# Optimization experiments

Hardware: AMD Instinct MI355X
Metric: run time of the kernel (lower is better)

Reference implementation:

```python
import jax, jax.numpy as jnp
import numpy as np

NUM_HEADS = 12

def _pe(L, d):
    # standard sinusoidal positional encoding, shape (1, L, d)
    pos = jnp.arange(L, dtype=jnp.float32)[:, None]
    i = jnp.arange(d)[None, :]
    angle = pos / jnp.power(10000.0, (2 * (i // 2)).astype(jnp.float32) / d)
    pe = jnp.where(i % 2 == 0, jnp.sin(angle), jnp.cos(angle))
    return pe[None]

def _ln(x, scale, bias, eps=1e-5):
    m = x.mean(-1, keepdims=True)
    v = ((x - m) ** 2).mean(-1, keepdims=True)
    return (x - m) / jnp.sqrt(v + eps) * scale + bias

def setup_inputs() -> dict:
    key = jax.random.key(0)
    ks = jax.random.split(key, 8)
    D = 768
    s = 0.02
    return {
        "x": jax.random.normal(ks[0], (8, D, 32, 32), jnp.float32),
        "context_token": jax.random.normal(ks[1], (1, 1, D), jnp.float32),
        "register_tokens": jax.random.normal(ks[2], (1, 4, D), jnp.float32),
        "in_proj_w": jax.random.normal(ks[3], (3 * D, D), jnp.float32) * s,
        "in_proj_b": jnp.zeros((3 * D,), jnp.float32),
        "out_proj_w": jax.random.normal(ks[4], (D, D), jnp.float32) * s,
        "out_proj_b": jnp.zeros((D,), jnp.float32),
        "ln1_s": jnp.ones((D,), jnp.float32),
        "ln1_b": jnp.zeros((D,), jnp.float32),
        "ln2_s": jnp.ones((D,), jnp.float32),
        "ln2_b": jnp.zeros((D,), jnp.float32),
        "ffn_w1": jax.random.normal(ks[5], (4 * D, D), jnp.float32) * s,
        "ffn_b1": jnp.zeros((4 * D,), jnp.float32),
        "ffn_w2": jax.random.normal(ks[6], (D, 4 * D), jnp.float32) * s,
        "ffn_b2": jnp.zeros((D,), jnp.float32),
    }

def reference(x, context_token, register_tokens, in_proj_w, in_proj_b,
              out_proj_w, out_proj_b, ln1_s, ln1_b, ln2_s, ln2_b,
              ffn_w1, ffn_b1, ffn_w2, ffn_b2):
    B, d, h, w = x.shape
    N = h * w
    R = register_tokens.shape[1]
    G = 1 + R  # global tokens: context + registers
    nh = NUM_HEADS
    dh = d // nh
    # (B, N, d)
    x_flat = x.reshape(B, d, N).transpose(0, 2, 1)
    tokens = jnp.concatenate([
        jnp.broadcast_to(context_token, (B, 1, d)),
        jnp.broadcast_to(register_tokens, (B, R, d)),
    ], axis=1)
    tokens = tokens + _pe(G, d)
    xwt = _ln(jnp.concatenate([tokens, x_flat], axis=1), ln1_s, ln1_b)
    S = G + N
    # MultiheadAttention (eval mode, dropout off): fused in-projection
    qkv = xwt @ in_proj_w.T + in_proj_b
    q, k, v = jnp.split(qkv, 3, axis=-1)
    to_heads = lambda t: t.reshape(B, S, nh, dh).transpose(0, 2, 1, 3)
    q, k, v = to_heads(q), to_heads(k), to_heads(v)
    scores = jnp.einsum('bhqd,bhkd->bhqk', q, k) / np.float32(np.sqrt(dh))
    # mask (True = disallowed): feature rows (>=G) cannot attend to global cols (<G);
    # global rows attend everything; feature-feature block allowed.
    row_feat = jnp.arange(S) >= G
    col_glob = jnp.arange(S) < G
    disallowed = row_feat[:, None] & col_glob[None, :]
    scores = jnp.where(disallowed, -jnp.inf, scores)
    attn = jax.nn.softmax(scores, axis=-1)
    o = jnp.einsum('bhqk,bhkd->bhqd', attn, v).transpose(0, 2, 1, 3).reshape(B, S, d)
    o = o @ out_proj_w.T + out_proj_b
    y = o + xwt
    ff = jax.nn.gelu(_ln(y, ln2_s, ln2_b) @ ffn_w1.T + ffn_b1, approximate=False) @ ffn_w2.T + ffn_b2
    y = y + ff
    context_out = y[:, 0:1, :]
    register_out = y[:, 1:G, :]
    feature_out = y[:, G:, :].transpose(0, 2, 1).reshape(B, d, h, w)
    return feature_out, context_out, register_out
```

## Files before the change

kernel.cpp:

```cpp
#include <hip/hip_runtime.h>
#include <hip/hip_bf16.h>
#include <cmath>

typedef unsigned short u16;
typedef __bf16 bf16x8 __attribute__((ext_vector_type(8)));
typedef float floatx4 __attribute__((ext_vector_type(4)));

#define SQ 1029
#define DM 768
#define NH 12
#define SQP 1088
#define SSC 0.18033688011112042f

#define GLD16(gp, lp) __builtin_amdgcn_global_load_lds( \
    (const __attribute__((address_space(1))) unsigned int*)(gp), \
    (__attribute__((address_space(3))) unsigned int*)(lp), 16, 0, 0)

#define OFF_WQKV ((size_t)0)
#define OFF_WOUT ((size_t)3538944)
#define OFF_W1   ((size_t)4718592)
#define OFF_W2   ((size_t)9437184)
#define OFF_XF   ((size_t)14155776)
#define OFF_XWT  ((size_t)26800128)
#define OFF_QKV  ((size_t)39444480)
#define OFF_VT   ((size_t)77783040)
#define OFF_Y    ((size_t)91152384)
#define OFF_BQ   ((size_t)103796736)

__device__ __forceinline__ float bf2f(u16 u) {
  unsigned int x = ((unsigned int)u) << 16;
  float f; __builtin_memcpy(&f, &x, 4); return f;
}
__device__ __forceinline__ u16 f2bf(float f) {
  unsigned int x; __builtin_memcpy(&x, &f, 4);
  x = (x + 0x7fffu + ((x >> 16) & 1u)) >> 16;
  return (u16)x;
}
__device__ __forceinline__ unsigned int pk_bf16(float a, float b) {
  __hip_bfloat162 h = __float22bfloat162_rn(make_float2(a, b));
  unsigned int u; __builtin_memcpy(&u, &h, 4); return u;
}

__device__ __forceinline__ void blockReduce2(float& s1, float& s2) {
  #pragma unroll
  for (int o = 32; o > 0; o >>= 1) { s1 += __shfl_xor(s1, o); s2 += __shfl_xor(s2, o); }
  __shared__ float t1[4], t2[4];
  const int w = threadIdx.x >> 6;
  if ((threadIdx.x & 63) == 0) { t1[w] = s1; t2[w] = s2; }
  __syncthreads();
  s1 = t1[0] + t1[1] + t1[2] + t1[3];
  s2 = t2[0] + t2[1] + t2[2] + t2[3];
}

__global__ __launch_bounds__(256) void convw_all(
    const float* __restrict__ a, const float* __restrict__ b,
    const float* __restrict__ c, const float* __restrict__ d,
    const float* __restrict__ bq, u16* __restrict__ dst, float* __restrict__ bqs) {
  int i = blockIdx.x * 256 + threadIdx.x;
  if (i >= 1770048) return;
  if (i >= 1769472) {
    const int off = i - 1769472;
    float4 v = ((const float4*)bq)[off];
    if (off < 192) { v.x *= SSC; v.y *= SSC; v.z *= SSC; v.w *= SSC; }
    ((float4*)bqs)[off] = v;
    return;
  }
  const float* src; int off;
  if (i < 442368)       { src = a; off = i; }
  else if (i < 589824)  { src = b; off = i - 442368; }
  else if (i < 1179648) { src = c; off = i - 589824; }
  else                  { src = d; off = i - 1179648; }
  float4 v = ((const float4*)src)[off];
  if (i < 147456) { v.x *= SSC; v.y *= SSC; v.z *= SSC; v.w *= SSC; }
  ushort4 o; o.x = f2bf(v.x); o.y = f2bf(v.y); o.z = f2bf(v.z); o.w = f2bf(v.w);
  ((ushort4*)dst)[i] = o;
}

__global__ __launch_bounds__(256) void ln1_fused(
    const float* __restrict__ x, const float* __restrict__ ctx, const float* __restrict__ regt,
    const float* __restrict__ g, const float* __restrict__ be, u16* __restrict__ xwt) {
  const int bx = blockIdx.x;
  const int tid = threadIdx.x;
  if (bx >= 256) {
    const int row = bx - 256;
    const int b = row / 5, s = row % 5;
    float v[3];
    #pragma unroll
    for (int i = 0; i < 3; ++i) {
      const int c = tid + i * 256;
      float tok = (s == 0) ? ctx[c] : regt[(s - 1) * DM + c];
      float e = (float)(2 * (c / 2)) * (1.0f / 768.0f);
      float ang = (float)s / powf(10000.0f, e);
      v[i] = tok + ((c & 1) ? cosf(ang) : sinf(ang));
    }
    float s1 = v[0] + v[1] + v[2];
    float s2 = v[0] * v[0] + v[1] * v[1] + v[2] * v[2];
    blockReduce2(s1, s2);
    const float mean = s1 * (1.0f / 768.0f);
    const float var = s2 * (1.0f / 768.0f) - mean * mean;
    const float rs = rsqrtf(fmaxf(var, 0.0f) + 1e-5f);
    #pragma unroll
    for (int i = 0; i < 3; ++i) {
      const int c = tid + i * 256;
      xwt[((size_t)b * SQ + s) * DM + c] = f2bf((v[i] - mean) * rs * g[c] + be[c]);
    }
    return;
  }
  __shared__ u16 XT[32][772];
  const int b = bx >> 5, st = bx & 31;
  const int i2 = tid & 15, cj = tid >> 4;
  const int n0 = st * 32;
  #pragma unroll 4
  for (int ct = 0; ct < 48; ++ct) {
    const int c = ct * 16 + cj;
    const float2 v = *(const float2*)&x[((size_t)b * 768 + c) * 1024 + n0 + i2 * 2];
    XT[i2 * 2][c]     = f2bf(v.x);
    XT[i2 * 2 + 1][c] = f2bf(v.y);
  }
  __syncthreads();
  const int wave = tid >> 6, lane = tid & 63;
  float gr[12], br[12];
  #pragma unroll
  for (int k = 0; k < 12; ++k) { gr[k] = g[lane + k * 64]; br[k] = be[lane + k * 64]; }
  #pragma unroll
  for (int rr = 0; rr < 8; ++rr) {
    const int row = wave * 8 + rr;
    float v[12];
    float s1 = 0.f, s2 = 0.f;
    #pragma unroll
    for (int k = 0; k < 12; ++k) {
      v[k] = bf2f(XT[row][lane + k * 64]);
      s1 += v[k]; s2 += v[k] * v[k];
    }
    #pragma unroll
    for (int o = 32; o > 0; o >>= 1) { s1 += __shfl_xor(s1, o); s2 += __shfl_xor(s2, o); }
    const float mean = s1 * (1.0f / 768.0f);
    const float var = s2 * (1.0f / 768.0f) - mean * mean;
    const float rs = rsqrtf(fmaxf(var, 0.0f) + 1e-5f);
    u16* dst = xwt + ((size_t)b * SQ + 5 + n0 + row) * DM;
    #pragma unroll
    for (int k = 0; k < 12; ++k)
      dst[lane + k * 64] = f2bf((v[k] - mean) * rs * gr[k] + br[k]);
  }
}

__global__ __launch_bounds__(256) void ln2k(
    const u16* __restrict__ y, const float* __restrict__ g, const float* __restrict__ be,
    u16* __restrict__ out) {
  const int row = blockIdx.x;
  const int tid = threadIdx.x;
  float v[3];
  #pragma unroll
  for (int i = 0; i < 3; ++i) v[i] = bf2f(y[(size_t)row * DM + tid + i * 256]);
  float s1 = v[0] + v[1] + v[2];
  float s2 = v[0] * v[0] + v[1] * v[1] + v[2] * v[2];
  blockReduce2(s1, s2);
  const float mean = s1 * (1.0f / 768.0f);
  const float var = s2 * (1.0f / 768.0f) - mean * mean;
  const float rs = rsqrtf(fmaxf(var, 0.0f) + 1e-5f);
  #pragma unroll
  for (int i = 0; i < 3; ++i) {
    const int c = tid + i * 256;
    out[(size_t)row * DM + c] = f2bf((v[i] - mean) * rs * g[c] + be[c]);
  }
}

template<int EPI, int K, int NB>
__global__ __launch_bounds__(256) void gemmk(
    const u16* __restrict__ A, const u16* __restrict__ W, const float* __restrict__ bias,
    const u16* __restrict__ res, u16* __restrict__ out, int M) {
  constexpr int N = NB * 128;
  __shared__ u16 SM[16384];
  u16* Asm = SM;
  u16* Bsm = SM + 8192;
  const int tid = threadIdx.x, wave = tid >> 6, lane = tid & 63, quad = lane >> 4, l16 = lane & 15;
  const int lin = blockIdx.x;
  constexpr int FULL = 64 * NB;
  int mb, nb;
  if (lin < FULL) { const int g = lin / (8 * NB); const int r = lin - g * 8 * NB; mb = g * 8 + (r & 7); nb = r >> 3; }
  else { mb = 64; nb = lin - FULL; }
  const int m0 = mb * 128, n0 = nb * 128;
  const int wm = wave & 1, wn = wave >> 1;

  const u16* Ap[4]; const u16* Wp[4]; u16* la[4]; u16* lb[4];
  #pragma unroll
  for (int it = 0; it < 4; ++it) {
    const int c = it * 256 + tid;
    const int row = c >> 3, gch = (c & 7) ^ (row & 7);
    Ap[it] = A + (size_t)min(m0 + row, M - 1) * K + gch * 8;
    Wp[it] = W + (size_t)(n0 + row) * K + gch * 8;
    la[it] = Asm + c * 8;
    lb[it] = Bsm + c * 8;
  }

  floatx4 acc[4][4];
  #pragma unroll
  for (int i = 0; i < 4; ++i)
    #pragma unroll
    for (int j = 0; j < 4; ++j) { floatx4 z = {0.f, 0.f, 0.f, 0.f}; acc[i][j] = z; }

  const int ch0 = (quad ^ (l16 & 7)) << 3;
  const int ch1 = ((4 + quad) ^ (l16 & 7)) << 3;

  #pragma unroll 1
  for (int ko = 0; ko < K / 768; ++ko) {
    #pragma unroll
    for (int ki = 0; ki < 768; ki += 64) {
      __syncthreads();
      #pragma unroll
      for (int it = 0; it < 4; ++it) GLD16(Ap[it] + ki, la[it]);
      #pragma unroll
      for (int it = 0; it < 4; ++it) GLD16(Wp[it] + ki, lb[it]);
      __syncthreads();
      #pragma unroll
      for (int kk = 0; kk < 2; ++kk) {
        const int ch = kk ? ch1 : ch0;
        bf16x8 a[4], b[4];
        #pragma unroll
        for (int i = 0; i < 4; ++i) a[i] = *(const bf16x8*)&Asm[(wm * 64 + i * 16 + l16) * 64 + ch];
        #pragma unroll
        for (int j = 0; j < 4; ++j) b[j] = *(const bf16x8*)&Bsm[(wn * 64 + j * 16 + l16) * 64 + ch];
        #pragma unroll
        for (int i = 0; i < 4; ++i)
          #pragma unroll
          for (int j = 0; j < 4; ++j)
            acc[i][j] = __builtin_amdgcn_mfma_f32_16x16x32_bf16(b[j], a[i], acc[i][j], 0, 0, 0);
      }
    }
    if (K > 768) {
      #pragma unroll
      for (int it = 0; it < 4; ++it) { Ap[it] += 768; Wp[it] += 768; }
    }
  }

  #pragma unroll
  for (int j = 0; j < 4; ++j) {
    const float4 b4 = *(const float4*)(bias + n0 + wn * 64 + j * 16 + quad * 4);
    #pragma unroll
    for (int i = 0; i < 4; ++i) {
      acc[i][j][0] += b4.x; acc[i][j][1] += b4.y; acc[i][j][2] += b4.z; acc[i][j][3] += b4.w;
    }
  }
  if constexpr (EPI == 2) {
    #pragma unroll
    for (int i = 0; i < 4; ++i)
      #pragma unroll
      for (int j = 0; j < 4; ++j)
        #pragma unroll
        for (int r = 0; r < 4; ++r) {
          const float v = acc[i][j][r];
          acc[i][j][r] = v / (1.0f + exp2f(-2.3022221f * (v + 0.044715f * v * v * v)));
        }
  }
  __syncthreads();
  u16* Ep = SM + wave * 2304;
  #pragma unroll
  for (int h = 0; h < 2; ++h) {
    #pragma unroll
    for (int i2 = 0; i2 < 2; ++i2) {
      const int i = h * 2 + i2;
      #pragma unroll
      for (int j = 0; j < 4; ++j) {
        uint2 w;
        w.x = pk_bf16(acc[i][j][0], acc[i][j][1]);
        w.y = pk_bf16(acc[i][j][2], acc[i][j][3]);
        *(uint2*)&Ep[(i2 * 16 + l16) * 72 + j * 16 + quad * 4] = w;
      }
    }
    #pragma unroll
    for (int s = 0; s < 4; ++s) {
      const int lrow = s * 8 + (lane >> 3);
      const int gm = m0 + wm * 64 + h * 32 + lrow;
      const int gn = n0 + wn * 64 + (lane & 7) * 8;
      uint4 lv = *(const uint4*)&Ep[lrow * 72 + (lane & 7) * 8];
      if constexpr (EPI == 1 || EPI == 3) {
        const uint4 rv = *(const uint4*)(res + (size_t)min(gm, M - 1) * N + gn);
        const unsigned* lp = &lv.x; const unsigned* rp = &rv.x;
        uint4 ov; unsigned* op = &ov.x;
        #pragma unroll
        for (int d = 0; d < 4; ++d) {
          const float a0 = bf2f((u16)(lp[d] & 0xffffu)) + bf2f((u16)(rp[d] & 0xffffu));
          const float a1 = bf2f((u16)(lp[d] >> 16)) + bf2f((u16)(rp[d] >> 16));
          op[d] = pk_bf16(a0, a1);
        }
        lv = ov;
      }
      if (gm < M) *(uint4*)(out + (size_t)gm * N + gn) = lv;
    }
  }
}

template<int EPI, int K, int NB>
__global__ __launch_bounds__(128, 2) void gemmw(
    const u16* __restrict__ A, const u16* __restrict__ W, const float* __restrict__ bias,
    const u16* __restrict__ res, u16* __restrict__ out, int M) {
  constexpr int N = NB * 128;
  __shared__ u16 SM[16384];
  u16* Asm = SM;
  u16* Bsm = SM + 8192;
  const int tid = threadIdx.x, wave = tid >> 6, lane = tid & 63, quad = lane >> 4, l16 = lane & 15;
  const int lin = blockIdx.x;
  constexpr int FULL = 64 * NB;
  int mb, nb;
  if (lin < FULL) { const int g = lin / (8 * NB); const int r = lin - g * 8 * NB; mb = g * 8 + (r & 7); nb = r >> 3; }
  else { mb = 64; nb = lin - FULL; }
  const int m0 = mb * 128, n0 = nb * 128;

  const u16* Ap[8]; const u16* Wp[8];
  #pragma unroll
  for (int it = 0; it < 8; ++it) {
    const int row = it * 16 + (tid >> 3);
    const int gch = (tid & 7) ^ (row & 7);
    Ap[it] = A + (size_t)min(m0 + row, M - 1) * K + gch * 8;
    Wp[it] = W + (size_t)(n0 + row) * K + gch * 8;
  }

  floatx4 acc[8][4];
  #pragma unroll
  for (int i = 0; i < 8; ++i)
    #pragma unroll
    for (int j = 0; j < 4; ++j) { floatx4 z = {0.f, 0.f, 0.f, 0.f}; acc[i][j] = z; }

  const int ch0 = (quad ^ (l16 & 7)) << 3;
  const int ch1 = ((4 + quad) ^ (l16 & 7)) << 3;

  #pragma unroll 1
  for (int ko = 0; ko < K / 768; ++ko) {
    #pragma unroll
    for (int ki = 0; ki < 768; ki += 64) {
      __syncthreads();
      #pragma unroll
      for (int it = 0; it < 8; ++it) GLD16(Ap[it] + ki, (char*)SM + (it * 128 + tid) * 16);
      #pragma unroll
      for (int it = 0; it < 8; ++it) GLD16(Wp[it] + ki, (char*)SM + 16384 + (it * 128 + tid) * 16);
      __syncthreads();
      #pragma unroll
      for (int kk = 0; kk < 2; ++kk) {
        const int ch = kk ? ch1 : ch0;
        bf16x8 a[8], b[4];
        #pragma unroll
        for (int i = 0; i < 8; ++i) a[i] = *(const bf16x8*)&Asm[(i * 16 + l16) * 64 + ch];
        #pragma unroll
        for (int j = 0; j < 4; ++j) b[j] = *(const bf16x8*)&Bsm[(wave * 64 + j * 16 + l16) * 64 + ch];
        #pragma unroll
        for (int i = 0; i < 8; ++i)
          #pragma unroll
          for (int j = 0; j < 4; ++j)
            acc[i][j] = __builtin_amdgcn_mfma_f32_16x16x32_bf16(b[j], a[i], acc[i][j], 0, 0, 0);
      }
    }
    if (K > 768) {
      #pragma unroll
      for (int it = 0; it < 8; ++it) { Ap[it] += 768; Wp[it] += 768; }
    }
  }

  #pragma unroll
  for (int j = 0; j < 4; ++j) {
    const float4 b4 = *(const float4*)(bias + n0 + wave * 64 + j * 16 + quad * 4);
    #pragma unroll
    for (int i = 0; i < 8; ++i) {
      acc[i][j][0] += b4.x; acc[i][j][1] += b4.y; acc[i][j][2] += b4.z; acc[i][j][3] += b4.w;
    }
  }
  if constexpr (EPI == 2) {
    #pragma unroll
    for (int i = 0; i < 8; ++i)
      #pragma unroll
      for (int j = 0; j < 4; ++j)
        #pragma unroll
        for (int r = 0; r < 4; ++r) {
          const float v = acc[i][j][r];
          acc[i][j][r] = v / (1.0f + exp2f(-2.3022221f * (v + 0.044715f * v * v * v)));
        }
  }
  __syncthreads();
  u16* Ep = SM + wave * 2304;
  #pragma unroll
  for (int g = 0; g < 4; ++g) {
    #pragma unroll
    for (int i2 = 0; i2 < 2; ++i2) {
      const int i = g * 2 + i2;
      #pragma unroll
      for (int j = 0; j < 4; ++j) {
        uint2 w;
        w.x = pk_bf16(acc[i][j][0], acc[i][j][1]);
        w.y = pk_bf16(acc[i][j][2], acc[i][j][3]);
        *(uint2*)&Ep[(i2 * 16 + l16) * 72 + j * 16 + quad * 4] = w;
      }
    }
    #pragma unroll
    for (int s = 0; s < 4; ++s) {
      const int lrow = s * 8 + (lane >> 3);
      const int gm = m0 + g * 32 + lrow;
      const int gn = n0 + wave * 64 + (lane & 7) * 8;
      uint4 lv = *(const uint4*)&Ep[lrow * 72 + (lane & 7) * 8];
      if constexpr (EPI == 1 || EPI == 3) {
        const uint4 rv = *(const uint4*)(res + (size_t)min(gm, M - 1) * N + gn);
        const unsigned* lp = &lv.x; const unsigned* rp = &rv.x;
        uint4 ov; unsigned* op = &ov.x;
        #pragma unroll
        for (int d = 0; d < 4; ++d) {
          const float a0 = bf2f((u16)(lp[d] & 0xffffu)) + bf2f((u16)(rp[d] & 0xffffu));
          const float a1 = bf2f((u16)(lp[d] >> 16)) + bf2f((u16)(rp[d] >> 16));
          op[d] = pk_bf16(a0, a1);
        }
        lv = ov;
      }
      if (gm < M) *(uint4*)(out + (size_t)gm * N + gn) = lv;
    }
  }
}

__global__ __launch_bounds__(256) void vtrans(const u16* __restrict__ qkv, u16* __restrict__ vt) {
  __shared__ u16 t[32][33];
  const int bh = blockIdx.x, st = blockIdx.y, dt = blockIdx.z;
  const int bq = bh / NH, hh = bh % NH;
  u16* vd = vt + (size_t)bh * 64 * SQP;
  const int i = threadIdx.x, jj = threadIdx.y;
  #pragma unroll
  for (int kk = 0; kk < 4; ++kk) {
    int j = jj + kk * 8;
    t[j][i] = qkv[(size_t)(bq * SQ + st * 32 + j) * 2304 + 1536 + hh * 64 + dt * 32 + i];
  }
  __syncthreads();
  #pragma unroll
  for (int kk = 0; kk < 4; ++kk) {
    int j = jj + kk * 8;
    vd[(size_t)(dt * 32 + j) * SQP + st * 32 + i] = t[i][j];
  }
}

__global__ __launch_bounds__(256) void attn_flash(
    const u16* __restrict__ qkv, const u16* __restrict__ vt, u16* __restrict__ out) {
  const int bh = blockIdx.x, qt = blockIdx.y;
  const int b = bh / NH, h = bh % NH;
  const int tid = threadIdx.x, wave = tid >> 6, lane = tid & 63, quad = lane >> 4, l16 = lane & 15;
  __shared__ u16 Qs[4096], Ks[4096], VTs[4096];
  __shared__ u16 Ps[64 * 72];
  const int q0 = qt * 64;
  const u16* qk = qkv + (size_t)b * SQ * 2304 + h * 64;
  const u16* vslab = vt + (size_t)bh * 64 * SQP;
  const int c0 = tid, c1 = tid + 256;
  const int r0 = c0 >> 3, q0c = (c0 & 7) ^ (r0 & 7);
  const int r1 = c1 >> 3, q1c = (c1 & 7) ^ (r1 & 7);
  u16* L0Q = Qs + wave * 512;  u16* L1Q = Qs + 2048 + wave * 512;
  u16* L0K = Ks + wave * 512;  u16* L1K = Ks + 2048 + wave * 512;
  u16* L0V = VTs + wave * 512; u16* L1V = VTs + 2048 + wave * 512;

  GLD16(qk + (size_t)(q0 + r0) * 2304 + q0c * 8, L0Q);
  GLD16(qk + (size_t)(q0 + r1) * 2304 + q1c * 8, L1Q);

  floatx4 Oa[4];
  #pragma unroll
  for (int nt = 0; nt < 4; ++nt) { floatx4 z = {0.f, 0.f, 0.f, 0.f}; Oa[nt] = z; }
  float l_acc = 0.f;
  const int qrow = wave * 16 + l16;
  const bool qfeat = (q0 + qrow >= 5);
  bf16x8 qf0, qf1;

  for (int t = 0; t < 17; ++t) {
    const int k0 = t * 64;
    __syncthreads();
    GLD16(qk + 768 + (size_t)(k0 + r0) * 2304 + q0c * 8, L0K);
    GLD16(qk + 768 + (size_t)(k0 + r1) * 2304 + q1c * 8, L1K);
    GLD16(vslab + (size_t)r0 * SQP + k0 + q0c * 8, L0V);
    GLD16(vslab + (size_t)r1 * SQP + k0 + q1c * 8, L1V);
    __syncthreads();

    if (t == 0) {
      qf0 = *(const bf16x8*)&Qs[qrow * 64 + ((quad ^ (qrow & 7)) << 3)];
      qf1 = *(const bf16x8*)&Qs[qrow * 64 + (((4 + quad) ^ (qrow & 7)) << 3)];
    }

    floatx4 st[4];
    #pragma unroll
    for (int mt = 0; mt < 4; ++mt) { floatx4 z = {0.f, 0.f, 0.f, 0.f}; st[mt] = z; }
    #pragma unroll
    for (int kk = 0; kk < 2; ++kk) {
      const bf16x8 qf = kk ? qf1 : qf0;
      #pragma unroll
      for (int mt = 0; mt < 4; ++mt) {
        const int krow = mt * 16 + l16;
        bf16x8 kf = *(const bf16x8*)&Ks[krow * 64 + (((kk * 4 + quad) ^ (krow & 7)) << 3)];
        st[mt] = __builtin_amdgcn_mfma_f32_16x16x32_bf16(kf, qf, st[mt], 0, 0, 0);
      }
    }

    if (t == 16) {
      float p[4];
      #pragma unroll
      for (int r = 0; r < 4; ++r) {
        float pv = exp2f(st[0][r]);
        p[r] = (quad * 4 + r < 5) ? pv : 0.f;
      }
      l_acc += (p[0] + p[1]) + (p[2] + p[3]);
      uint2 w;
      w.x = pk_bf16(p[0], p[1]);
      w.y = pk_bf16(p[2], p[3]);
      *(uint2*)&Ps[qrow * 72 + quad * 4] = w;
      const uint2 zz = {0u, 0u};
      #pragma unroll
      for (int mt = 1; mt < 4; ++mt) *(uint2*)&Ps[qrow * 72 + mt * 16 + quad * 4] = zz;
    } else if (t == 0) {
      #pragma unroll
      for (int mt = 0; mt < 4; ++mt) {
        float p[4];
        #pragma unroll
        for (int r = 0; r < 4; ++r) {
          float pv = exp2f(st[mt][r]);
          if (mt == 0) pv = (qfeat && (quad * 4 + r < 5)) ? 0.f : pv;
          p[r] = pv;
        }
        l_acc += (p[0] + p[1]) + (p[2] + p[3]);
        uint2 w;
        w.x = pk_bf16(p[0], p[1]);
        w.y = pk_bf16(p[2], p[3]);
        *(uint2*)&Ps[qrow * 72 + mt * 16 + quad * 4] = w;
      }
    } else {
      #pragma unroll
      for (int mt = 0; mt < 4; ++mt) {
        float p[4];
        #pragma unroll
        for (int r = 0; r < 4; ++r) p[r] = exp2f(st[mt][r]);
        l_acc += (p[0] + p[1]) + (p[2] + p[3]);
        uint2 w;
        w.x = pk_bf16(p[0], p[1]);
        w.y = pk_bf16(p[2], p[3]);
        *(uint2*)&Ps[qrow * 72 + mt * 16 + quad * 4] = w;
      }
    }

    auto pv_step = [&](int kk) {
      bf16x8 pf = *(const bf16x8*)&Ps[qrow * 72 + kk * 32 + quad * 8];
      #pragma unroll
      for (int nt = 0; nt < 4; ++nt) {
        const int brow = nt * 16 + l16;
        bf16x8 bb = *(const bf16x8*)&VTs[brow * 64 + (((kk * 4 + quad) ^ (brow & 7)) << 3)];
        Oa[nt] = __builtin_amdgcn_mfma_f32_16x16x32_bf16(pf, bb, Oa[nt], 0, 0, 0);
      }
    };
    pv_step(0);
    if (t != 16) pv_step(1);
  }

  float lt = l_acc;
  lt += __shfl_xor(lt, 16);
  lt += __shfl_xor(lt, 32);
  lt = fmaxf(lt, 1e-30f);
  #pragma unroll
  for (int nt = 0; nt < 4; ++nt)
    #pragma unroll
    for (int r = 0; r < 4; ++r) {
      const int qo = quad * 4 + r;
      const float lr = __shfl(lt, (lane & 48) | qo);
      const int qg2 = q0 + wave * 16 + qo;
      if (qg2 < SQ)
        out[((size_t)b * SQ + qg2) * DM + h * 64 + nt * 16 + l16] = f2bf(Oa[nt][r] / lr);
    }
}

__global__ __launch_bounds__(256) void transpose_out(const u16* __restrict__ yf, float* __restrict__ out) {
  const int bx = blockIdx.x;
  const int tid = threadIdx.x;
  if (bx >= 6144) {
    const int idx = (bx - 6144) * 256 + tid;
    if (idx >= 8 * 5 * DM) return;
    const int b = idx / (5 * DM);
    const int r = idx % (5 * DM);
    const int s = r / DM, c = r % DM;
    const float v = bf2f(yf[((size_t)b * SQ + s) * DM + c]);
    if (s == 0) out[(size_t)6291456 + (size_t)b * DM + c] = v;
    else out[(size_t)6291456 + 6144 + ((size_t)b * 4 + (s - 1)) * DM + c] = v;
    return;
  }
  __shared__ u16 tile[32][33];
  const int b = bx / 768, rr = bx % 768, nt = rr / 24, ct = rr % 24;
  const int i = tid & 31, jj = tid >> 5;
  #pragma unroll
  for (int kk = 0; kk < 4; ++kk) {
    int j = jj + kk * 8;
    tile[j][i] = yf[((size_t)b * SQ + 5 + nt * 32 + j) * DM + ct * 32 + i];
  }
  __syncthreads();
  #pragma unroll
  for (int kk = 0; kk < 4; ++kk) {
    int j = jj + kk * 8;
    out[((size_t)b * 768 + ct * 32 + j) * 1024 + nt * 32 + i] = bf2f(tile[i][j]);
  }
}

extern "C" void kernel_launch(void* const* d_in, const int* in_sizes, int n_in,
                              void* d_out, int out_size, void* d_ws, size_t ws_size,
                              hipStream_t stream) {
  const float* x    = (const float*)d_in[0];
  const float* ctx  = (const float*)d_in[1];
  const float* regt = (const float*)d_in[2];
  const float* wqkv = (const float*)d_in[3];
  const float* bqkv = (const float*)d_in[4];
  const float* wout = (const float*)d_in[5];
  const float* bout = (const float*)d_in[6];
  const float* ln1s = (const float*)d_in[7];
  const float* ln1b = (const float*)d_in[8];
  const float* ln2s = (const float*)d_in[9];
  const float* ln2b = (const float*)d_in[10];
  const float* w1   = (const float*)d_in[11];
  const float* b1   = (const float*)d_in[12];
  const float* w2   = (const float*)d_in[13];
  const float* b2   = (const float*)d_in[14];

  char* ws = (char*)d_ws;
  u16* wb_all = (u16*)(ws + OFF_WQKV);
  u16* wqkv_b = (u16*)(ws + OFF_WQKV);
  u16* wout_b = (u16*)(ws + OFF_WOUT);
  u16* w1_b   = (u16*)(ws + OFF_W1);
  u16* w2_b   = (u16*)(ws + OFF_W2);
  u16* xwt    = (u16*)(ws + OFF_XWT);
  u16* qkv    = (u16*)(ws + OFF_QKV);
  u16* vtb    = (u16*)(ws + OFF_VT);
  u16* yb     = (u16*)(ws + OFF_Y);
  float* bqs  = (float*)(ws + OFF_BQ);
  u16* attnb  = (u16*)(ws + OFF_XF);
  u16* ynorm  = (u16*)(ws + OFF_XF);
  u16* h1     = (u16*)(ws + OFF_QKV);
  u16* yfin   = (u16*)(ws + OFF_XWT);
  float* outp = (float*)d_out;

  convw_all   <<<6915, 256, 0, stream>>>(wqkv, wout, w1, w2, bqkv, wb_all, bqs);
  ln1_fused   <<<296, 256, 0, stream>>>(x, ctx, regt, ln1s, ln1b, xwt);
  gemmw<0, 768, 18><<<65 * 18, 128, 0, stream>>>(xwt, wqkv_b, bqs, nullptr, qkv, 8232);
  vtrans      <<<dim3(96, 34, 2), dim3(32, 8), 0, stream>>>(qkv, vtb);
  attn_flash  <<<dim3(96, 17), 256, 0, stream>>>(qkv, vtb, attnb);
  gemmk<1, 768, 6><<<65 * 6, 256, 0, stream>>>(attnb, wout_b, bout, xwt, yb, 8232);
  ln2k        <<<8232, 256, 0, stream>>>(yb, ln2s, ln2b, ynorm);
  gemmw<2, 768, 24><<<65 * 24, 128, 0, stream>>>(ynorm, w1_b, b1, nullptr, h1, 8232);
  gemmk<3, 3072, 6><<<65 * 6, 256, 0, stream>>>(h1, w2_b, b2, yb, yfin, 8232);
  transpose_out<<<6264, 256, 0, stream>>>(yfin, outp);
}
```

Baseline: 384.8 us.

## Process two query tiles per attention block and vectorize LN2 per wave

The attention kernel now handles 128 queries per block, in two 64-row halves, so each K/V tile loaded into shared memory is reused twice. This halves K/V global traffic and the grid drops from 17 to 9 query tiles. Q fragments are read straight from global memory instead of being staged through shared memory. Separately, LN2 now assigns one row per wavefront, uses vectorized loads and stores and a shuffle-only reduction, with 4 rows per block. The cost is fewer blocks in flight and more registers for two accumulator sets, which may lower occupancy.

```diff
diff --git a/kernel.cpp b/kernel.cpp
--- a/kernel.cpp
+++ b/kernel.cpp
@@ -147,21 +147,35 @@
 __global__ __launch_bounds__(256) void ln2k(
     const u16* __restrict__ y, const float* __restrict__ g, const float* __restrict__ be,
     u16* __restrict__ out) {
-  const int row = blockIdx.x;
-  const int tid = threadIdx.x;
-  float v[3];
-  #pragma unroll
-  for (int i = 0; i < 3; ++i) v[i] = bf2f(y[(size_t)row * DM + tid + i * 256]);
-  float s1 = v[0] + v[1] + v[2];
-  float s2 = v[0] * v[0] + v[1] * v[1] + v[2] * v[2];
-  blockReduce2(s1, s2);
+  const int row = blockIdx.x * 4 + (threadIdx.x >> 6);
+  const int lane = threadIdx.x & 63;
+  const u16* src = y + (size_t)row * DM;
+  float v[12];
+  float s1 = 0.f, s2 = 0.f;
+  #pragma unroll
+  for (int k = 0; k < 3; ++k) {
+    const ushort4 u = *(const ushort4*)&src[k * 256 + lane * 4];
+    const float a0 = bf2f(u.x), a1 = bf2f(u.y), a2 = bf2f(u.z), a3 = bf2f(u.w);
+    v[k * 4 + 0] = a0; v[k * 4 + 1] = a1; v[k * 4 + 2] = a2; v[k * 4 + 3] = a3;
+    s1 += (a0 + a1) + (a2 + a3);
+    s2 += (a0 * a0 + a1 * a1) + (a2 * a2 + a3 * a3);
+  }
+  #pragma unroll
+  for (int o = 32; o > 0; o >>= 1) { s1 += __shfl_xor(s1, o); s2 += __shfl_xor(s2, o); }
   const float mean = s1 * (1.0f / 768.0f);
   const float var = s2 * (1.0f / 768.0f) - mean * mean;
   const float rs = rsqrtf(fmaxf(var, 0.0f) + 1e-5f);
-  #pragma unroll
-  for (int i = 0; i < 3; ++i) {
-    const int c = tid + i * 256;
-    out[(size_t)row * DM + c] = f2bf((v[i] - mean) * rs * g[c] + be[c]);
+  u16* dst = out + (size_t)row * DM;
+  #pragma unroll
+  for (int k = 0; k < 3; ++k) {
+    const float4 g4 = *(const float4*)&g[k * 256 + lane * 4];
+    const float4 b4 = *(const float4*)&be[k * 256 + lane * 4];
+    uint2 w;
+    w.x = pk_bf16((v[k * 4 + 0] - mean) * rs * g4.x + b4.x,
+                  (v[k * 4 + 1] - mean) * rs * g4.y + b4.y);
+    w.y = pk_bf16((v[k * 4 + 2] - mean) * rs * g4.z + b4.z,
+                  (v[k * 4 + 3] - mean) * rs * g4.w + b4.w);
+    *(uint2*)&dst[k * 256 + lane * 4] = w;
   }
 }
 
@@ -436,57 +450,35 @@
   const int bh = blockIdx.x, qt = blockIdx.y;
   const int b = bh / NH, h = bh % NH;
   const int tid = threadIdx.x, wave = tid >> 6, lane = tid & 63, quad = lane >> 4, l16 = lane & 15;
-  __shared__ u16 Qs[4096], Ks[4096], VTs[4096];
-  __shared__ u16 Ps[64 * 72];
-  const int q0 = qt * 64;
+  __shared__ u16 Ks[4096], VTs[4096];
+  __shared__ u16 Ps[128 * 72];
+  const int q0 = qt * 128;
+  const bool two = (qt < 8);
   const u16* qk = qkv + (size_t)b * SQ * 2304 + h * 64;
   const u16* vslab = vt + (size_t)bh * 64 * SQP;
-  const int c0 = tid, c1 = tid + 256;
-  const int r0 = c0 >> 3, q0c = (c0 & 7) ^ (r0 & 7);
-  const int r1 = c1 >> 3, q1c = (c1 & 7) ^ (r1 & 7);
-  u16* L0Q = Qs + wave * 512;  u16* L1Q = Qs + 2048 + wave * 512;
+  const int r0 = tid >> 3,          q0c = (tid & 7) ^ (r0 & 7);
+  const int r1 = (tid + 256) >> 3,  q1c = (tid & 7) ^ (r1 & 7);
   u16* L0K = Ks + wave * 512;  u16* L1K = Ks + 2048 + wave * 512;
   u16* L0V = VTs + wave * 512; u16* L1V = VTs + 2048 + wave * 512;
 
-  GLD16(qk + (size_t)(q0 + r0) * 2304 + q0c * 8, L0Q);
-  GLD16(qk + (size_t)(q0 + r1) * 2304 + q1c * 8, L1Q);
-
-  floatx4 Oa[4];
-  #pragma unroll
-  for (int nt = 0; nt < 4; ++nt) { floatx4 z = {0.f, 0.f, 0.f, 0.f}; Oa[nt] = z; }
-  float l_acc = 0.f;
   const int qrow = wave * 16 + l16;
-  const bool qfeat = (q0 + qrow >= 5);
-  bf16x8 qf0, qf1;
-
-  for (int t = 0; t < 17; ++t) {
-    const int k0 = t * 64;
-    __syncthreads();
-    GLD16(qk + 768 + (size_t)(k0 + r0) * 2304 + q0c * 8, L0K);
-    GLD16(qk + 768 + (size_t)(k0 + r1) * 2304 + q1c * 8, L1K);
-    GLD16(vslab + (size_t)r0 * SQP + k0 + q0c * 8, L0V);
-    GLD16(vslab + (size_t)r1 * SQP + k0 + q1c * 8, L1V);
-    __syncthreads();
-
-    if (t == 0) {
-      qf0 = *(const bf16x8*)&Qs[qrow * 64 + ((quad ^ (qrow & 7)) << 3)];
-      qf1 = *(const bf16x8*)&Qs[qrow * 64 + (((4 + quad) ^ (qrow & 7)) << 3)];
-    }
-
-    floatx4 st[4];
-    #pragma unroll
-    for (int mt = 0; mt < 4; ++mt) { floatx4 z = {0.f, 0.f, 0.f, 0.f}; st[mt] = z; }
-    #pragma unroll
-    for (int kk = 0; kk < 2; ++kk) {
-      const bf16x8 qf = kk ? qf1 : qf0;
-      #pragma unroll
-      for (int mt = 0; mt < 4; ++mt) {
-        const int krow = mt * 16 + l16;
-        bf16x8 kf = *(const bf16x8*)&Ks[krow * 64 + (((kk * 4 + quad) ^ (krow & 7)) << 3)];
-        st[mt] = __builtin_amdgcn_mfma_f32_16x16x32_bf16(kf, qf, st[mt], 0, 0, 0);
-      }
-    }
-
+  const bf16x8 qf0 = *(const bf16x8*)&qk[(size_t)(q0 + qrow) * 2304 + quad * 8];
+  const bf16x8 qf1 = *(const bf16x8*)&qk[(size_t)(q0 + qrow) * 2304 + (4 + quad) * 8];
+  bf16x8 qf2 = qf0, qf3 = qf1;
+  if (two) {
+    qf2 = *(const bf16x8*)&qk[(size_t)(q0 + 64 + qrow) * 2304 + quad * 8];
+    qf3 = *(const bf16x8*)&qk[(size_t)(q0 + 64 + qrow) * 2304 + (4 + quad) * 8];
+  }
+
+  floatx4 Oa0[4], Oa1[4];
+  #pragma unroll
+  for (int nt = 0; nt < 4; ++nt) {
+    floatx4 z = {0.f, 0.f, 0.f, 0.f}; Oa0[nt] = z; Oa1[nt] = z;
+  }
+  float l0 = 0.f, l1 = 0.f;
+  const bool qfeat0 = (q0 + qrow >= 5);
+
+  auto sm_store = [&](floatx4* st, bool qfeat, int prow, float& l_acc, int t) {
     if (t == 16) {
       float p[4];
       #pragma unroll
@@ -498,10 +490,10 @@
       uint2 w;
       w.x = pk_bf16(p[0], p[1]);
       w.y = pk_bf16(p[2], p[3]);
-      *(uint2*)&Ps[qrow * 72 + quad * 4] = w;
+      *(uint2*)&Ps[prow * 72 + quad * 4] = w;
       const uint2 zz = {0u, 0u};
       #pragma unroll
-      for (int mt = 1; mt < 4; ++mt) *(uint2*)&Ps[qrow * 72 + mt * 16 + quad * 4] = zz;
+      for (int mt = 1; mt < 4; ++mt) *(uint2*)&Ps[prow * 72 + mt * 16 + quad * 4] = zz;
     } else if (t == 0) {
       #pragma unroll
       for (int mt = 0; mt < 4; ++mt) {
@@ -516,7 +508,7 @@
         uint2 w;
         w.x = pk_bf16(p[0], p[1]);
         w.y = pk_bf16(p[2], p[3]);
-        *(uint2*)&Ps[qrow * 72 + mt * 16 + quad * 4] = w;
+        *(uint2*)&Ps[prow * 72 + mt * 16 + quad * 4] = w;
       }
     } else {
       #pragma unroll
@@ -528,37 +520,99 @@
         uint2 w;
         w.x = pk_bf16(p[0], p[1]);
         w.y = pk_bf16(p[2], p[3]);
-        *(uint2*)&Ps[qrow * 72 + mt * 16 + quad * 4] = w;
-      }
-    }
-
-    auto pv_step = [&](int kk) {
-      bf16x8 pf = *(const bf16x8*)&Ps[qrow * 72 + kk * 32 + quad * 8];
+        *(uint2*)&Ps[prow * 72 + mt * 16 + quad * 4] = w;
+      }
+    }
+  };
+  auto pv_acc = [&](floatx4* Oa, int prow, int t) {
+    #pragma unroll
+    for (int kk = 0; kk < 2; ++kk) {
+      if (kk == 1 && t == 16) break;
+      bf16x8 pf = *(const bf16x8*)&Ps[prow * 72 + kk * 32 + quad * 8];
       #pragma unroll
       for (int nt = 0; nt < 4; ++nt) {
         const int brow = nt * 16 + l16;
         bf16x8 bb = *(const bf16x8*)&VTs[brow * 64 + (((kk * 4 + quad) ^ (brow & 7)) << 3)];
         Oa[nt] = __builtin_amdgcn_mfma_f32_16x16x32_bf16(pf, bb, Oa[nt], 0, 0, 0);
       }
-    };
-    pv_step(0);
-    if (t != 16) pv_step(1);
-  }
-
-  float lt = l_acc;
-  lt += __shfl_xor(lt, 16);
-  lt += __shfl_xor(lt, 32);
-  lt = fmaxf(lt, 1e-30f);
-  #pragma unroll
-  for (int nt = 0; nt < 4; ++nt)
-    #pragma unroll
-    for (int r = 0; r < 4; ++r) {
-      const int qo = quad * 4 + r;
-      const float lr = __shfl(lt, (lane & 48) | qo);
-      const int qg2 = q0 + wave * 16 + qo;
-      if (qg2 < SQ)
-        out[((size_t)b * SQ + qg2) * DM + h * 64 + nt * 16 + l16] = f2bf(Oa[nt][r] / lr);
-    }
+    }
+  };
+
+  for (int t = 0; t < 17; ++t) {
+    const int k0 = t * 64;
+    __syncthreads();
+    GLD16(qk + 768 + (size_t)(k0 + r0) * 2304 + q0c * 8, L0K);
+    GLD16(qk + 768 + (size_t)(k0 + r1) * 2304 + q1c * 8, L1K);
+    GLD16(vslab + (size_t)r0 * SQP + k0 + q0c * 8, L0V);
+    GLD16(vslab + (size_t)r1 * SQP + k0 + q1c * 8, L1V);
+    __syncthreads();
+
+    floatx4 st[4];
+    #pragma unroll
+    for (int mt = 0; mt < 4; ++mt) { floatx4 z = {0.f, 0.f, 0.f, 0.f}; st[mt] = z; }
+    #pragma unroll
+    for (int kk = 0; kk < 2; ++kk) {
+      const bf16x8 qf = kk ? qf1 : qf0;
+      #pragma unroll
+      for (int mt = 0; mt < 4; ++mt) {
+        const int krow = mt * 16 + l16;
+        bf16x8 kf = *(const bf16x8*)&Ks[krow * 64 + (((kk * 4 + quad) ^ (krow & 7)) << 3)];
+        st[mt] = __builtin_amdgcn_mfma_f32_16x16x32_bf16(kf, qf, st[mt], 0, 0, 0);
+      }
+    }
+    sm_store(st, qfeat0, qrow, l0, t);
+    pv_acc(Oa0, qrow, t);
+
+    if (two) {
+      #pragma unroll
+      for (int mt = 0; mt < 4; ++mt) { floatx4 z = {0.f, 0.f, 0.f, 0.f}; st[mt] = z; }
+      #pragma unroll
+      for (int kk = 0; kk < 2; ++kk) {
+        const bf16x8 qf = kk ? qf3 : qf2;
+        #pragma unroll
+        for (int mt = 0; mt < 4; ++mt) {
+          const int krow = mt * 16 + l16;
+          bf16x8 kf = *(const bf16x8*)&Ks[krow * 64 + (((kk * 4 + quad) ^ (krow & 7)) << 3)];
+          st[mt] = __builtin_amdgcn_mfma_f32_16x16x32_bf16(kf, qf, st[mt], 0, 0, 0);
+        }
+      }
+      sm_store(st, true, 64 + qrow, l1, t);
+      pv_acc(Oa1, 64 + qrow, t);
+    }
+  }
+
+  {
+    float lt = l0;
+    lt += __shfl_xor(lt, 16);
+    lt += __shfl_xor(lt, 32);
+    lt = fmaxf(lt, 1e-30f);
+    #pragma unroll
+    for (int nt = 0; nt < 4; ++nt)
+      #pragma unroll
+      for (int r = 0; r < 4; ++r) {
+        const int qo = quad * 4 + r;
+        const float lr = __shfl(lt, (lane & 48) | qo);
+        const int qg = q0 + wave * 16 + qo;
+        if (qg < SQ)
+          out[((size_t)b * SQ + qg) * DM + h * 64 + nt * 16 + l16] = f2bf(Oa0[nt][r] / lr);
+      }
+  }
+  if (two) {
+    float lt = l1;
+    lt += __shfl_xor(lt, 16);
+    lt += __shfl_xor(lt, 32);
+    lt = fmaxf(lt, 1e-30f);
+    #pragma unroll
+    for (int nt = 0; nt < 4; ++nt)
+      #pragma unroll
+      for (int r = 0; r < 4; ++r) {
+        const int qo = quad * 4 + r;
+        const float lr = __shfl(lt, (lane & 48) | qo);
+        const int qg = q0 + 64 + wave * 16 + qo;
+        if (qg < SQ)
+          out[((size_t)b * SQ + qg) * DM + h * 64 + nt * 16 + l16] = f2bf(Oa1[nt][r] / lr);
+      }
+  }
 }
 
 __global__ __launch_bounds__(256) void transpose_out(const u16* __restrict__ yf, float* __restrict__ out) {
@@ -631,9 +685,9 @@
   ln1_fused   <<<296, 256, 0, stream>>>(x, ctx, regt, ln1s, ln1b, xwt);
   gemmw<0, 768, 18><<<65 * 18, 128, 0, stream>>>(xwt, wqkv_b, bqs, nullptr, qkv, 8232);
   vtrans      <<<dim3(96, 34, 2), dim3(32, 8), 0, stream>>>(qkv, vtb);
-  attn_flash  <<<dim3(96, 17), 256, 0, stream>>>(qkv, vtb, attnb);
+  attn_flash  <<<dim3(96, 9), 256, 0, stream>>>(qkv, vtb, attnb);
   gemmk<1, 768, 6><<<65 * 6, 256, 0, stream>>>(attnb, wout_b, bout, xwt, yb, 8232);
-  ln2k        <<<8232, 256, 0, stream>>>(yb, ln2s, ln2b, ynorm);
+  ln2k        <<<2058, 256, 0, stream>>>(yb, ln2s, ln2b, ynorm);
   gemmw<2, 768, 24><<<65 * 24, 128, 0, stream>>>(ynorm, w1_b, b1, nullptr, h1, 8232);
   gemmk<3, 3072, 6><<<65 * 6, 256, 0, stream>>>(h1, w2_b, b2, yb, yfin, 8232);
   transpose_out<<<6264, 256, 0, stream>>>(yfin, outp);
```

Measured after the change: 394.7 us. 2.6% more time.
